# Optimization experiments

Measured on AMD Instinct MI355X. Metric: run time of the kernel, lower is better.

The kernel has to match this reference:

```python
import jax, jax.numpy as jnp
import numpy as np
from jax import lax

B, C, IC, H, W = 4, 64, 32, 64, 64


def _conv(x, w, b, stride, pad):
    y = lax.conv_general_dilated(
        x, w, (stride, stride), [(pad, pad), (pad, pad)],
        dimension_numbers=('NCHW', 'OIHW', 'NCHW'))
    return y + b[None, :, None, None]


def setup_inputs() -> dict:
    key = jax.random.key(0)
    ks = jax.random.split(key, 15)
    s = 0.05
    inp = {
        'x': jax.random.normal(ks[0], (B, C, H, W), jnp.float32),
        # GEunit convs (3x3)
        'd1_w': jax.random.normal(ks[1], (C, C, 3, 3), jnp.float32) * s,
        'd1_b': jax.random.normal(ks[2], (C,), jnp.float32) * s,
        'd2_w': jax.random.normal(ks[3], (C, C, 3, 3), jnp.float32) * s,
        'd2_b': jax.random.normal(ks[4], (C,), jnp.float32) * s,
        'd3_w': jax.random.normal(ks[5], (C, C, 3, 3), jnp.float32) * s,
        'd3_b': jax.random.normal(ks[6], (C,), jnp.float32) * s,
        # 1x1 projections
        'g_w': jax.random.normal(ks[7], (IC, C, 1, 1), jnp.float32) * s,
        'g_b': jax.random.normal(ks[8], (IC,), jnp.float32) * s,
        'th_w': jax.random.normal(ks[9], (IC, C, 1, 1), jnp.float32) * s,
        'th_b': jax.random.normal(ks[10], (IC,), jnp.float32) * s,
        'ph_w': jax.random.normal(ks[11], (IC, C, 1, 1), jnp.float32) * s,
        'ph_b': jax.random.normal(ks[12], (IC,), jnp.float32) * s,
        # output projection (zero-init in original; random here for nontrivial baseline)
        'w_w': jax.random.normal(ks[13], (C, IC, 1, 1), jnp.float32) * s,
        'w_b': jax.random.normal(ks[14], (C,), jnp.float32) * s,
    }
    return inp


def _forward(x, d1_w, d1_b, d2_w, d2_b, d3_w, d3_b,
             g_w, g_b, th_w, th_b, ph_w, ph_b, w_w, w_b):
    lrelu = lambda v: jnp.where(v >= 0, v, 0.2 * v)
    y = lrelu(_conv(x, d1_w, d1_b, 2, 1))
    y = lrelu(_conv(y, d2_w, d2_b, 2, 1))
    y = _conv(y, d3_w, d3_b, 2, 1)
    y = jax.image.resize(y, (x.shape[0], x.shape[1], x.shape[2], x.shape[3]),
                         method='bilinear')  # align_corners=False equivalent
    am = jax.nn.sigmoid(y) * x  # attention_map, [B,C,H,W]

    b, c, h, w = am.shape
    n = h * w
    g_x = _conv(am, g_w, g_b, 1, 0).reshape(b, IC, n)      # [B,IC,N]
    theta = _conv(am, th_w, th_b, 1, 0).reshape(b, IC, n)  # [B,IC,N]
    phi = _conv(am, ph_w, ph_b, 1, 0).reshape(b, IC, n)    # [B,IC,N]

    # f[b,i,j] = theta[:, i] . phi[:, j];  softmax over dim=1 (the i axis)
    f = jnp.einsum('bci,bcj->bij', theta, phi)             # [B,N,N]
    f_div_C = jax.nn.softmax(f, axis=1)
    y2 = jnp.einsum('bij,bjc->bic', f_div_C, g_x.transpose(0, 2, 1))  # [B,N,IC]
    y2 = y2.transpose(0, 2, 1).reshape(b, IC, h, w)

    W_y = _conv(y2, w_w, w_b, 1, 0)
    z = W_y + am
    return z * x


def reference(x, d1_w, d1_b, d2_w, d2_b, d3_w, d3_b,
              g_w, g_b, th_w, th_b, ph_w, ph_b, w_w, w_b):
    return _forward(x, d1_w, d1_b, d2_w, d2_b, d3_w, d3_b,
                    g_w, g_b, th_w, th_b, ph_w, ph_b, w_w, w_b)
```

## Files before the change

kernel.cpp:

```cpp
#include <hip/hip_runtime.h>

#define B_ 4
#define C_ 64
#define IC_ 32
#define N_ 4096
#define LOG2E 1.44269504088896341f

typedef __attribute__((ext_vector_type(8))) short short8;
typedef __attribute__((ext_vector_type(4))) float floatx4;
typedef unsigned short ushort_t;

__device__ __forceinline__ unsigned short f2bf(float f) {
  unsigned u = __float_as_uint(f);
  u += 0x7FFFu + ((u >> 16) & 1u);
  return (unsigned short)(u >> 16);
}
__device__ __forceinline__ float bf2f(unsigned short h) {
  return __uint_as_float(((unsigned)h) << 16);
}

__global__ void __launch_bounds__(256) pack_xw_k(
    const float* __restrict__ x, unsigned short* __restrict__ xclp,
    const float* __restrict__ d1_w, const float* __restrict__ d2_w, const float* __restrict__ d3_w,
    const float* __restrict__ th_w, const float* __restrict__ ph_w, const float* __restrict__ g_w,
    const float* __restrict__ th_b, const float* __restrict__ ph_b, const float* __restrict__ g_b,
    unsigned short* __restrict__ wpk, unsigned short* __restrict__ wproj, float* __restrict__ bproj)
{
  __shared__ float s[64][65];
  const int t = threadIdx.x;
  if (blockIdx.x < 256) {
    const int b = blockIdx.x >> 6, h = blockIdx.x & 63;
    for (int idx = t; idx < 4096; idx += 256) {
      int c = idx >> 6, w = idx & 63;
      s[c][w] = x[((size_t)(b * 64 + c)) * 4096 + h * 64 + w];
    }
    __syncthreads();
    for (int idx = t; idx < 4096; idx += 256) {
      int w = idx >> 6, c = idx & 63;
      xclp[(((size_t)b * 66 + h + 1) * 66 + (w + 1)) * 64 + c] = f2bf(s[c][w]);
    }
  } else {
    const int tid = (blockIdx.x - 256) * 256 + t;
    for (int idx = tid; idx < 3 * 36864; idx += 16 * 256) {
      int cv = idx / 36864, r = idx % 36864;
      int tap = r / 4096, r2 = r % 4096;
      int oc = r2 >> 6, ic = r2 & 63;
      const float* src = (cv == 0) ? d1_w : (cv == 1) ? d2_w : d3_w;
      wpk[(size_t)cv * 36864 + tap * 4096 + oc * 64 + ic] = f2bf(src[oc * 576 + ic * 9 + tap]);
    }
    for (int idx = tid; idx < 6144; idx += 16 * 256) {
      int m = idx >> 6, ic = idx & 63;
      float v = (m < 32) ? LOG2E * th_w[m * 64 + ic]
              : (m < 64) ? ph_w[(m - 32) * 64 + ic]
                         : g_w[(m - 64) * 64 + ic];
      wproj[m * 64 + ic] = f2bf(v);
    }
    for (int m = tid; m < 96; m += 16 * 256) {
      bproj[m] = (m < 32) ? LOG2E * th_b[m] : (m < 64) ? ph_b[m - 32] : g_b[m - 64];
    }
  }
}

template<int IN_PW, int OUT_H, bool LRELU, bool OUT_BF16>
__global__ void __launch_bounds__(64) convmf_k(
    const unsigned short* __restrict__ xin, const unsigned short* __restrict__ wp,
    const float* __restrict__ bias, unsigned short* __restrict__ obf,
    float* __restrict__ of32)
{
  constexpr int NTILES = OUT_H * OUT_H / 16;
  const int lane = threadIdx.x;
  const int n15 = lane & 15, quad = lane >> 4;
  int bx = blockIdx.x;
  const int octile = bx & 3; bx >>= 2;
  const int otile = bx % NTILES;
  const int b = bx / NTILES;
  const int o = otile * 16 + n15;
  const int oh = o / OUT_H, ow = o % OUT_H;
  const unsigned short* xb = xin + (size_t)b * IN_PW * IN_PW * 64;
  floatx4 acc = {0.f, 0.f, 0.f, 0.f};
#pragma unroll
  for (int tap = 0; tap < 9; ++tap) {
    const int kh = tap / 3, kw = tap % 3;
    const unsigned short* xpix = xb + ((size_t)(oh * 2 + kh) * IN_PW + (ow * 2 + kw)) * 64;
#pragma unroll
    for (int ks = 0; ks < 2; ++ks) {
      short8 af = *reinterpret_cast<const short8*>(
          wp + ((size_t)tap * 64 + octile * 16 + n15) * 64 + ks * 32 + quad * 8);
      short8 bf = *reinterpret_cast<const short8*>(xpix + ks * 32 + quad * 8);
      acc = __builtin_amdgcn_mfma_f32_16x16x32_bf16(af, bf, acc, 0, 0, 0);
    }
  }
  const float4 bv = *reinterpret_cast<const float4*>(bias + octile * 16 + quad * 4);
  float v[4] = {acc[0] + bv.x, acc[1] + bv.y, acc[2] + bv.z, acc[3] + bv.w};
  if (LRELU) {
#pragma unroll
    for (int r = 0; r < 4; ++r) v[r] = (v[r] >= 0.f) ? v[r] : 0.2f * v[r];
  }
  if (OUT_BF16) {
    constexpr int OPW = OUT_H + 2;
    unsigned short pk[4];
#pragma unroll
    for (int r = 0; r < 4; ++r) pk[r] = f2bf(v[r]);
    *reinterpret_cast<uint2*>(
        obf + (((size_t)b * OPW + oh + 1) * OPW + (ow + 1)) * 64 + octile * 16 + quad * 4) =
        *reinterpret_cast<uint2*>(pk);
  } else {
    *reinterpret_cast<float4*>(
        of32 + ((size_t)b * OUT_H * OUT_H + o) * 64 + octile * 16 + quad * 4) =
        *reinterpret_cast<float4*>(v);
  }
}

__global__ void __launch_bounds__(256) upsproj_k(
    const float* __restrict__ y3cl, const float* __restrict__ x,
    const unsigned short* __restrict__ wproj, const float* __restrict__ bproj,
    unsigned short* __restrict__ am_cl, unsigned short* __restrict__ thph,
    unsigned short* __restrict__ g16)
{
  const int b = blockIdx.x >> 6, oh = blockIdx.x & 63;
  const int t = threadIdx.x;
  __shared__ float s0[512], s1[512];
  __shared__ unsigned short s_am[64][72];
  float sh = (oh + 0.5f) * 0.125f - 0.5f;
  float fh = floorf(sh); float ah = sh - fh; int h0 = (int)fh;
  int h0c = min(7, max(0, h0)), h1c = min(7, max(0, h0 + 1));
  const float* yb = y3cl + (size_t)b * 4096;
  for (int i = t; i < 512; i += 256) { s0[i] = yb[h0c * 512 + i]; s1[i] = yb[h1c * 512 + i]; }
  __syncthreads();
  {
    const int ow = t >> 2, cq = t & 3;
    float sw = (ow + 0.5f) * 0.125f - 0.5f;
    float fw = floorf(sw); float aw = sw - fw; int w0 = (int)fw;
    int w0c = min(7, max(0, w0)), w1c = min(7, max(0, w0 + 1));
    const int n = oh * 64 + ow;
    const float* xb = x + (size_t)b * 64 * 4096 + n;
    unsigned short* ap = am_cl + ((size_t)b * N_ + n) * 64 + cq * 16;
#pragma unroll
    for (int u = 0; u < 4; ++u) {
      int c0 = cq * 16 + u * 4;
      float4 a00 = *reinterpret_cast<const float4*>(&s0[w0c * 64 + c0]);
      float4 a01 = *reinterpret_cast<const float4*>(&s0[w1c * 64 + c0]);
      float4 a10 = *reinterpret_cast<const float4*>(&s1[w0c * 64 + c0]);
      float4 a11 = *reinterpret_cast<const float4*>(&s1[w1c * 64 + c0]);
      float i0[4] = {a00.x * (1.f - aw) + a01.x * aw, a00.y * (1.f - aw) + a01.y * aw,
                     a00.z * (1.f - aw) + a01.z * aw, a00.w * (1.f - aw) + a01.w * aw};
      float i1[4] = {a10.x * (1.f - aw) + a11.x * aw, a10.y * (1.f - aw) + a11.y * aw,
                     a10.z * (1.f - aw) + a11.z * aw, a10.w * (1.f - aw) + a11.w * aw};
      unsigned short pk[4];
#pragma unroll
      for (int vi = 0; vi < 4; ++vi) {
        float vv = i0[vi] * (1.f - ah) + i1[vi] * ah;
        float xv = xb[(size_t)(c0 + vi) * 4096];
        float sig = 1.f / (1.f + __expf(-vv));
        pk[vi] = f2bf(sig * xv);
      }
      uint2 pkt = *reinterpret_cast<uint2*>(pk);
      *reinterpret_cast<uint2*>(ap + u * 4) = pkt;
      *reinterpret_cast<uint2*>(&s_am[ow][c0]) = pkt;
    }
  }
  __syncthreads();
  const int wave = t >> 6, lane = t & 63;
  const int n15 = lane & 15, quad = lane >> 4;
  const int n = oh * 64 + wave * 16 + n15;
  const unsigned short* srow = &s_am[wave * 16 + n15][0];
  const short8 bf0 = *reinterpret_cast<const short8*>(srow + quad * 8);
  const short8 bf1 = *reinterpret_cast<const short8*>(srow + 32 + quad * 8);
#pragma unroll
  for (int mt = 0; mt < 6; ++mt) {
    short8 a0 = *reinterpret_cast<const short8*>(wproj + ((size_t)mt * 16 + n15) * 64 + quad * 8);
    short8 a1 = *reinterpret_cast<const short8*>(wproj + ((size_t)mt * 16 + n15) * 64 + 32 + quad * 8);
    floatx4 acc = {0.f, 0.f, 0.f, 0.f};
    acc = __builtin_amdgcn_mfma_f32_16x16x32_bf16(a0, bf0, acc, 0, 0, 0);
    acc = __builtin_amdgcn_mfma_f32_16x16x32_bf16(a1, bf1, acc, 0, 0, 0);
    const float4 bv = *reinterpret_cast<const float4*>(bproj + mt * 16 + quad * 4);
    float v[4] = {acc[0] + bv.x, acc[1] + bv.y, acc[2] + bv.z, acc[3] + bv.w};
    if (mt < 4) {
      unsigned short pk[4];
#pragma unroll
      for (int r = 0; r < 4; ++r) pk[r] = f2bf(v[r]);
      *reinterpret_cast<uint2*>(thph + ((size_t)b * N_ + n) * 64 + mt * 16 + quad * 4) =
          *reinterpret_cast<uint2*>(pk);
    } else {
#pragma unroll
      for (int r = 0; r < 4; ++r)
        g16[((size_t)b * 32 + (mt - 4) * 16 + quad * 4 + r) * N_ + n] = f2bf(v[r]);
    }
  }
}

__global__ void __launch_bounds__(256) attn_stats_k(
    const unsigned short* __restrict__ thph, float* __restrict__ lpart)
{
  const int b  = blockIdx.y;
  const int iz = blockIdx.z;
  const int t = threadIdx.x, wave = t >> 6, lane = t & 63;
  const int n15 = lane & 15, quad = lane >> 4;
  const int jw = blockIdx.x * 256 + wave * 64;
  const unsigned short* base = thph + (size_t)b * N_ * 64;
  short8 bv[4];
#pragma unroll
  for (int v = 0; v < 4; ++v)
    bv[v] = *reinterpret_cast<const short8*>(base + (size_t)(jw + v * 16 + n15) * 64 + 32 + quad * 8);
  float ls[4] = {0.f, 0.f, 0.f, 0.f};
  const unsigned short* ap = base + (size_t)(iz * 256 + n15) * 64 + quad * 8;
  short8 ac = *reinterpret_cast<const short8*>(ap);
  for (int st = 0; st < 16; ++st) {
    short8 an = *reinterpret_cast<const short8*>(ap + (size_t)((st < 15) ? st + 1 : st) * 1024);
#pragma unroll
    for (int v = 0; v < 4; ++v) {
      floatx4 z = {0.f, 0.f, 0.f, 0.f};
      z = __builtin_amdgcn_mfma_f32_16x16x32_bf16(ac, bv[v], z, 0, 0, 0);
      ls[v] += (__builtin_amdgcn_exp2f(z[0]) + __builtin_amdgcn_exp2f(z[1]))
             + (__builtin_amdgcn_exp2f(z[2]) + __builtin_amdgcn_exp2f(z[3]));
    }
    ac = an;
  }
#pragma unroll
  for (int v = 0; v < 4; ++v) {
    ls[v] += __shfl_xor(ls[v], 16);
    ls[v] += __shfl_xor(ls[v], 32);
  }
  if (quad == 0) {
#pragma unroll
    for (int v = 0; v < 4; ++v)
      lpart[((size_t)iz * B_ + b) * N_ + jw + v * 16 + n15] = ls[v];
  }
}

__global__ void __launch_bounds__(256) scale_g_k(
    const float* __restrict__ lpart, unsigned short* __restrict__ g16)
{
  const int b = blockIdx.y;
  const int c0 = blockIdx.z * 8;
  const int j = blockIdx.x * 256 + threadIdx.x;
  float l = 0.f;
#pragma unroll
  for (int iz = 0; iz < 16; ++iz) l += lpart[((size_t)iz * B_ + b) * N_ + j];
  const float rl = 1.f / l;
  unsigned short* gp = g16 + ((size_t)b * 32 + c0) * N_ + j;
#pragma unroll
  for (int c = 0; c < 8; ++c) {
    gp[(size_t)c * N_] = f2bf(bf2f(gp[(size_t)c * N_]) * rl);
  }
}

#define PHI_PITCH 40
#define G_PITCH   136
__global__ void __launch_bounds__(256, 4) attn_pv_k(
    const unsigned short* __restrict__ thph, const unsigned short* __restrict__ g16,
    unsigned short* __restrict__ y2p)
{
  const int b  = blockIdx.y;
  const int jq = blockIdx.z;
  const int t = threadIdx.x, wave = t >> 6, lane = t & 63;
  const int n15 = lane & 15, quad = lane >> 4;
  const int iw = blockIdx.x * 64 + wave * 16;
  const unsigned short* base = thph + (size_t)b * N_ * 64;
  const unsigned short* gs   = g16  + (size_t)b * 32 * N_;
  __shared__ unsigned short phi_lds[2][128 * PHI_PITCH];
  __shared__ unsigned short g_lds[2][32 * G_PITCH];

  const short8 bth = *reinterpret_cast<const short8*>(base + (size_t)(iw + n15) * 64 + quad * 8);
  floatx4 Y0 = {0.f, 0.f, 0.f, 0.f}, Y1 = {0.f, 0.f, 0.f, 0.f};

  const int rphi = wave * 32 + (lane >> 2), cph = lane & 3;
  const int cg   = wave * 8  + (lane >> 4), chg = lane & 15;

  uint4 sp0, sp1, sg0, sg1;
  const int jbase = jq * 1024;
  sp0 = *reinterpret_cast<const uint4*>(base + (size_t)(jbase + rphi) * 64 + 32 + cph * 8);
  sp1 = *reinterpret_cast<const uint4*>(base + (size_t)(jbase + rphi + 16) * 64 + 32 + cph * 8);
  sg0 = *reinterpret_cast<const uint4*>(gs + (size_t)cg * N_ + jbase + chg * 8);
  sg1 = *reinterpret_cast<const uint4*>(gs + (size_t)(cg + 4) * N_ + jbase + chg * 8);
  *reinterpret_cast<uint4*>(&phi_lds[0][rphi * PHI_PITCH + cph * 8]) = sp0;
  *reinterpret_cast<uint4*>(&phi_lds[0][(rphi + 16) * PHI_PITCH + cph * 8]) = sp1;
  *reinterpret_cast<uint4*>(&g_lds[0][cg * G_PITCH + chg * 8]) = sg0;
  *reinterpret_cast<uint4*>(&g_lds[0][(cg + 4) * G_PITCH + chg * 8]) = sg1;
  __syncthreads();

  int j0 = jbase;
  for (int ch = 0; ch < 8; ++ch, j0 += 128) {
    const int cur = ch & 1;
    if (ch < 7) {
      const int jn = j0 + 128;
      sp0 = *reinterpret_cast<const uint4*>(base + (size_t)(jn + rphi) * 64 + 32 + cph * 8);
      sp1 = *reinterpret_cast<const uint4*>(base + (size_t)(jn + rphi + 16) * 64 + 32 + cph * 8);
      sg0 = *reinterpret_cast<const uint4*>(gs + (size_t)cg * N_ + jn + chg * 8);
      sg1 = *reinterpret_cast<const uint4*>(gs + (size_t)(cg + 4) * N_ + jn + chg * 8);
    }
    const unsigned short* phb = &phi_lds[cur][0];
    const unsigned short* glb = &g_lds[cur][0];
    unsigned pk[8][2];
#pragma unroll
    for (int jt = 0; jt < 8; ++jt) {
      short8 aph = *reinterpret_cast<const short8*>(phb + (jt * 16 + n15) * PHI_PITCH + quad * 8);
      floatx4 z = {0.f, 0.f, 0.f, 0.f};
      z = __builtin_amdgcn_mfma_f32_16x16x32_bf16(aph, bth, z, 0, 0, 0);
      float e0 = __builtin_amdgcn_exp2f(z[0]), e1 = __builtin_amdgcn_exp2f(z[1]);
      float e2 = __builtin_amdgcn_exp2f(z[2]), e3 = __builtin_amdgcn_exp2f(z[3]);
      pk[jt][0] = __builtin_amdgcn_perm(__float_as_uint(e1), __float_as_uint(e0), 0x07060302);
      pk[jt][1] = __builtin_amdgcn_perm(__float_as_uint(e3), __float_as_uint(e2), 0x07060302);
    }
#pragma unroll
    for (int sg = 0; sg < 4; ++sg) {
      union { unsigned u[4]; short8 v; } pa, gb0, gb1;
      pa.u[0] = pk[2 * sg][0];     pa.u[1] = pk[2 * sg][1];
      pa.u[2] = pk[2 * sg + 1][0]; pa.u[3] = pk[2 * sg + 1][1];
      const unsigned short* gr0 = glb + n15 * G_PITCH + sg * 32 + quad * 4;
      const unsigned short* gr1 = glb + (16 + n15) * G_PITCH + sg * 32 + quad * 4;
      uint2 lo0 = *reinterpret_cast<const uint2*>(gr0);
      uint2 hi0 = *reinterpret_cast<const uint2*>(gr0 + 16);
      uint2 lo1 = *reinterpret_cast<const uint2*>(gr1);
      uint2 hi1 = *reinterpret_cast<const uint2*>(gr1 + 16);
      gb0.u[0] = lo0.x; gb0.u[1] = lo0.y; gb0.u[2] = hi0.x; gb0.u[3] = hi0.y;
      gb1.u[0] = lo1.x; gb1.u[1] = lo1.y; gb1.u[2] = hi1.x; gb1.u[3] = hi1.y;
      Y0 = __builtin_amdgcn_mfma_f32_16x16x32_bf16(pa.v, gb0.v, Y0, 0, 0, 0);
      Y1 = __builtin_amdgcn_mfma_f32_16x16x32_bf16(pa.v, gb1.v, Y1, 0, 0, 0);
    }
    if (ch < 7) {
      const int nb = cur ^ 1;
      *reinterpret_cast<uint4*>(&phi_lds[nb][rphi * PHI_PITCH + cph * 8]) = sp0;
      *reinterpret_cast<uint4*>(&phi_lds[nb][(rphi + 16) * PHI_PITCH + cph * 8]) = sp1;
      *reinterpret_cast<uint4*>(&g_lds[nb][cg * G_PITCH + chg * 8]) = sg0;
      *reinterpret_cast<uint4*>(&g_lds[nb][(cg + 4) * G_PITCH + chg * 8]) = sg1;
    }
    __syncthreads();
  }
  unsigned w0[2], w1[2];
  w0[0] = ((unsigned)f2bf(Y0[1]) << 16) | f2bf(Y0[0]);
  w0[1] = ((unsigned)f2bf(Y0[3]) << 16) | f2bf(Y0[2]);
  w1[0] = ((unsigned)f2bf(Y1[1]) << 16) | f2bf(Y1[0]);
  w1[1] = ((unsigned)f2bf(Y1[3]) << 16) | f2bf(Y1[2]);
  *reinterpret_cast<uint2*>(
      y2p + (((size_t)jq * B_ + b) * 32 + n15) * N_ + iw + quad * 4) =
      *reinterpret_cast<uint2*>(w0);
  *reinterpret_cast<uint2*>(
      y2p + (((size_t)jq * B_ + b) * 32 + 16 + n15) * N_ + iw + quad * 4) =
      *reinterpret_cast<uint2*>(w1);
}

__global__ void __launch_bounds__(256) final_k(
    const unsigned short* __restrict__ y2p, const float* __restrict__ w_w,
    const float* __restrict__ w_b, const unsigned short* __restrict__ am_cl,
    const float* __restrict__ x, float* __restrict__ out)
{
  const int n0 = (blockIdx.x * 256 + threadIdx.x) * 2;
  const int o0 = blockIdx.y * 8;
  const int b  = blockIdx.z;
  float a0[8], a1[8];
#pragma unroll
  for (int u = 0; u < 8; ++u) { a0[u] = w_b[o0 + u]; a1[u] = a0[u]; }
  for (int c = 0; c < 32; ++c) {
    float s0 = 0.f, s1 = 0.f;
#pragma unroll
    for (int ph = 0; ph < 4; ++ph) {
      unsigned v = *reinterpret_cast<const unsigned*>(
          y2p + (((size_t)ph * B_ + b) * 32 + c) * N_ + n0);
      s0 += bf2f((unsigned short)(v & 0xffffu));
      s1 += bf2f((unsigned short)(v >> 16));
    }
#pragma unroll
    for (int u = 0; u < 8; ++u) {
      float wv = w_w[(o0 + u) * 32 + c];
      a0[u] += wv * s0; a1[u] += wv * s1;
    }
  }
  const short8 am0 = *reinterpret_cast<const short8*>(am_cl + ((size_t)b * N_ + n0) * 64 + o0);
  const short8 am1 = *reinterpret_cast<const short8*>(am_cl + ((size_t)b * N_ + n0 + 1) * 64 + o0);
#pragma unroll
  for (int u = 0; u < 8; ++u) {
    size_t off = ((size_t)b * 64 + o0 + u) * N_ + n0;
    float2 xv = *reinterpret_cast<const float2*>(x + off);
    float2 ov;
    ov.x = (a0[u] + bf2f((unsigned short)am0[u])) * xv.x;
    ov.y = (a1[u] + bf2f((unsigned short)am1[u])) * xv.y;
    *reinterpret_cast<float2*>(out + off) = ov;
  }
}

extern "C" void kernel_launch(void* const* d_in, const int* in_sizes, int n_in,
                              void* d_out, int out_size, void* d_ws, size_t ws_size,
                              hipStream_t stream) {
  const float* x    = (const float*)d_in[0];
  const float* d1_w = (const float*)d_in[1];
  const float* d1_b = (const float*)d_in[2];
  const float* d2_w = (const float*)d_in[3];
  const float* d2_b = (const float*)d_in[4];
  const float* d3_w = (const float*)d_in[5];
  const float* d3_b = (const float*)d_in[6];
  const float* g_w  = (const float*)d_in[7];
  const float* g_b  = (const float*)d_in[8];
  const float* th_w = (const float*)d_in[9];
  const float* th_b = (const float*)d_in[10];
  const float* ph_w = (const float*)d_in[11];
  const float* ph_b = (const float*)d_in[12];
  const float* w_w  = (const float*)d_in[13];
  const float* w_b  = (const float*)d_in[14];
  float* out = (float*)d_out;

  char* p = (char*)d_ws;
  unsigned short* am_cl = (unsigned short*)p;  p += (size_t)B_ * N_ * 64 * 2;
  unsigned short* thph  = (unsigned short*)p;  p += (size_t)B_ * N_ * 64 * 2;
  unsigned short* g16   = (unsigned short*)p;  p += (size_t)B_ * 32 * N_ * 2;
  float* lpart          = (float*)p;           p += (size_t)16 * B_ * N_ * 4;
  unsigned short* y2p   = (unsigned short*)p;  p += (size_t)4 * B_ * 32 * N_ * 2;
  float* y3cl           = (float*)p;           p += (size_t)B_ * 64 * 64 * 4;
  unsigned short* wpk   = (unsigned short*)p;  p += (size_t)3 * 36864 * 2;
  unsigned short* wproj = (unsigned short*)p;  p += (size_t)96 * 64 * 2;
  float* bproj          = (float*)p;           p += (size_t)96 * 4;
  char* zbase = p;
  unsigned short* xclp  = (unsigned short*)p;  p += (size_t)B_ * 66 * 66 * 64 * 2;
  unsigned short* y1clp = (unsigned short*)p;  p += (size_t)B_ * 34 * 34 * 64 * 2;
  unsigned short* y2clp = (unsigned short*)p;  p += (size_t)B_ * 18 * 18 * 64 * 2;
  const size_t zbytes = (size_t)(p - zbase);

  hipMemsetAsync(zbase, 0, zbytes, stream);
  pack_xw_k<<<272, 256, 0, stream>>>(x, xclp, d1_w, d2_w, d3_w, th_w, ph_w, g_w,
                                     th_b, ph_b, g_b, wpk, wproj, bproj);
  convmf_k<66, 32, true,  true ><<<1024, 64, 0, stream>>>(xclp,  wpk,             d1_b, y1clp, nullptr);
  convmf_k<34, 16, true,  true ><<<256,  64, 0, stream>>>(y1clp, wpk + 36864,     d2_b, y2clp, nullptr);
  convmf_k<18,  8, false, false><<<64,   64, 0, stream>>>(y2clp, wpk + 2 * 36864, d3_b, nullptr, y3cl);
  upsproj_k<<<256, 256, 0, stream>>>(y3cl, x, wproj, bproj, am_cl, thph, g16);
  attn_stats_k<<<dim3(16, 4, 16), 256, 0, stream>>>(thph, lpart);
  scale_g_k<<<dim3(16, 4, 4), 256, 0, stream>>>(lpart, g16);
  attn_pv_k<<<dim3(64, 4, 4), 256, 0, stream>>>(thph, g16, y2p);
  final_k<<<dim3(8, 8, 4), 256, 0, stream>>>(y2p, w_w, w_b, am_cl, x, out);
}
```

Before: 153.8 us.

## Split conv K across waves with LDS reduction; stage theta tile in LDS

```diff
diff --git a/kernel.cpp b/kernel.cpp
--- a/kernel.cpp
+++ b/kernel.cpp
@@ -8,7 +8,6 @@
 
 typedef __attribute__((ext_vector_type(8))) short short8;
 typedef __attribute__((ext_vector_type(4))) float floatx4;
-typedef unsigned short ushort_t;
 
 __device__ __forceinline__ unsigned short f2bf(float f) {
   unsigned u = __float_as_uint(f);
@@ -62,18 +61,17 @@
 }
 
 template<int IN_PW, int OUT_H, bool LRELU, bool OUT_BF16>
-__global__ void __launch_bounds__(64) convmf_k(
+__global__ void __launch_bounds__(512) convmf_k(
     const unsigned short* __restrict__ xin, const unsigned short* __restrict__ wp,
     const float* __restrict__ bias, unsigned short* __restrict__ obf,
     float* __restrict__ of32)
 {
   constexpr int NTILES = OUT_H * OUT_H / 16;
-  const int lane = threadIdx.x;
+  const int t = threadIdx.x, lane = t & 63, wave = t >> 6;
+  const int octile = wave & 3, ks = wave >> 2;
   const int n15 = lane & 15, quad = lane >> 4;
-  int bx = blockIdx.x;
-  const int octile = bx & 3; bx >>= 2;
-  const int otile = bx % NTILES;
-  const int b = bx / NTILES;
+  const int otile = blockIdx.x % NTILES;
+  const int b = blockIdx.x / NTILES;
   const int o = otile * 16 + n15;
   const int oh = o / OUT_H, ow = o % OUT_H;
   const unsigned short* xb = xin + (size_t)b * IN_PW * IN_PW * 64;
@@ -82,32 +80,38 @@
   for (int tap = 0; tap < 9; ++tap) {
     const int kh = tap / 3, kw = tap % 3;
     const unsigned short* xpix = xb + ((size_t)(oh * 2 + kh) * IN_PW + (ow * 2 + kw)) * 64;
-#pragma unroll
-    for (int ks = 0; ks < 2; ++ks) {
-      short8 af = *reinterpret_cast<const short8*>(
-          wp + ((size_t)tap * 64 + octile * 16 + n15) * 64 + ks * 32 + quad * 8);
-      short8 bf = *reinterpret_cast<const short8*>(xpix + ks * 32 + quad * 8);
-      acc = __builtin_amdgcn_mfma_f32_16x16x32_bf16(af, bf, acc, 0, 0, 0);
-    }
-  }
-  const float4 bv = *reinterpret_cast<const float4*>(bias + octile * 16 + quad * 4);
-  float v[4] = {acc[0] + bv.x, acc[1] + bv.y, acc[2] + bv.z, acc[3] + bv.w};
-  if (LRELU) {
-#pragma unroll
-    for (int r = 0; r < 4; ++r) v[r] = (v[r] >= 0.f) ? v[r] : 0.2f * v[r];
-  }
-  if (OUT_BF16) {
-    constexpr int OPW = OUT_H + 2;
-    unsigned short pk[4];
-#pragma unroll
-    for (int r = 0; r < 4; ++r) pk[r] = f2bf(v[r]);
-    *reinterpret_cast<uint2*>(
-        obf + (((size_t)b * OPW + oh + 1) * OPW + (ow + 1)) * 64 + octile * 16 + quad * 4) =
-        *reinterpret_cast<uint2*>(pk);
-  } else {
-    *reinterpret_cast<float4*>(
-        of32 + ((size_t)b * OUT_H * OUT_H + o) * 64 + octile * 16 + quad * 4) =
-        *reinterpret_cast<float4*>(v);
+    short8 af = *reinterpret_cast<const short8*>(
+        wp + ((size_t)tap * 64 + octile * 16 + n15) * 64 + ks * 32 + quad * 8);
+    short8 bf = *reinterpret_cast<const short8*>(xpix + ks * 32 + quad * 8);
+    acc = __builtin_amdgcn_mfma_f32_16x16x32_bf16(af, bf, acc, 0, 0, 0);
+  }
+  __shared__ float red[4][64][4];
+  if (ks == 1) {
+#pragma unroll
+    for (int r = 0; r < 4; ++r) red[octile][lane][r] = acc[r];
+  }
+  __syncthreads();
+  if (ks == 0) {
+    const float4 bv = *reinterpret_cast<const float4*>(bias + octile * 16 + quad * 4);
+    float v[4];
+#pragma unroll
+    for (int r = 0; r < 4; ++r) {
+      v[r] = acc[r] + red[octile][lane][r] + ((const float*)&bv)[r];
+      if (LRELU) v[r] = (v[r] >= 0.f) ? v[r] : 0.2f * v[r];
+    }
+    if (OUT_BF16) {
+      constexpr int OPW = OUT_H + 2;
+      unsigned short pk[4];
+#pragma unroll
+      for (int r = 0; r < 4; ++r) pk[r] = f2bf(v[r]);
+      *reinterpret_cast<uint2*>(
+          obf + (((size_t)b * OPW + oh + 1) * OPW + (ow + 1)) * 64 + octile * 16 + quad * 4) =
+          *reinterpret_cast<uint2*>(pk);
+    } else {
+      *reinterpret_cast<float4*>(
+          of32 + ((size_t)b * OUT_H * OUT_H + o) * 64 + octile * 16 + quad * 4) =
+          *reinterpret_cast<float4*>(v);
+    }
   }
 }
 
@@ -189,6 +193,7 @@
   }
 }
 
+#define TH_PITCH 40
 __global__ void __launch_bounds__(256) attn_stats_k(
     const unsigned short* __restrict__ thph, float* __restrict__ lpart)
 {
@@ -198,15 +203,24 @@
   const int n15 = lane & 15, quad = lane >> 4;
   const int jw = blockIdx.x * 256 + wave * 64;
   const unsigned short* base = thph + (size_t)b * N_ * 64;
+  __shared__ unsigned short th[256 * TH_PITCH];
+#pragma unroll
+  for (int it = 0; it < 4; ++it) {
+    int idx = it * 256 + t;
+    int row = idx >> 2, ck = idx & 3;
+    *reinterpret_cast<uint4*>(&th[row * TH_PITCH + ck * 8]) =
+        *reinterpret_cast<const uint4*>(base + (size_t)(iz * 256 + row) * 64 + ck * 8);
+  }
   short8 bv[4];
 #pragma unroll
   for (int v = 0; v < 4; ++v)
     bv[v] = *reinterpret_cast<const short8*>(base + (size_t)(jw + v * 16 + n15) * 64 + 32 + quad * 8);
+  __syncthreads();
   float ls[4] = {0.f, 0.f, 0.f, 0.f};
-  const unsigned short* ap = base + (size_t)(iz * 256 + n15) * 64 + quad * 8;
-  short8 ac = *reinterpret_cast<const short8*>(ap);
+  short8 ac = *reinterpret_cast<const short8*>(&th[n15 * TH_PITCH + quad * 8]);
   for (int st = 0; st < 16; ++st) {
-    short8 an = *reinterpret_cast<const short8*>(ap + (size_t)((st < 15) ? st + 1 : st) * 1024);
+    const int rn = ((st < 15) ? st + 1 : st) * 16 + n15;
+    short8 an = *reinterpret_cast<const short8*>(&th[rn * TH_PITCH + quad * 8]);
 #pragma unroll
     for (int v = 0; v < 4; ++v) {
       floatx4 z = {0.f, 0.f, 0.f, 0.f};
@@ -418,9 +432,9 @@
   hipMemsetAsync(zbase, 0, zbytes, stream);
   pack_xw_k<<<272, 256, 0, stream>>>(x, xclp, d1_w, d2_w, d3_w, th_w, ph_w, g_w,
                                      th_b, ph_b, g_b, wpk, wproj, bproj);
-  convmf_k<66, 32, true,  true ><<<1024, 64, 0, stream>>>(xclp,  wpk,             d1_b, y1clp, nullptr);
-  convmf_k<34, 16, true,  true ><<<256,  64, 0, stream>>>(y1clp, wpk + 36864,     d2_b, y2clp, nullptr);
-  convmf_k<18,  8, false, false><<<64,   64, 0, stream>>>(y2clp, wpk + 2 * 36864, d3_b, nullptr, y3cl);
+  convmf_k<66, 32, true,  true ><<<256, 512, 0, stream>>>(xclp,  wpk,             d1_b, y1clp, nullptr);
+  convmf_k<34, 16, true,  true ><<<64,  512, 0, stream>>>(y1clp, wpk + 36864,     d2_b, y2clp, nullptr);
+  convmf_k<18,  8, false, false><<<16,  512, 0, stream>>>(y2clp, wpk + 2 * 36864, d3_b, nullptr, y3cl);
   upsproj_k<<<256, 256, 0, stream>>>(y3cl, x, wproj, bproj, am_cl, thph, g16);
   attn_stats_k<<<dim3(16, 4, 16), 256, 0, stream>>>(thph, lpart);
   scale_g_k<<<dim3(16, 4, 4), 256, 0, stream>>>(lpart, g16);
```

New measurement: 160.3 us. +4.2%, slower.

## Fuse attention stats, g scaling and PV into one persistent kernel with grid barriers

Applied to the files above, without the earlier changes.

```diff
diff --git a/kernel.cpp b/kernel.cpp
--- a/kernel.cpp
+++ b/kernel.cpp
@@ -5,10 +5,10 @@
 #define IC_ 32
 #define N_ 4096
 #define LOG2E 1.44269504088896341f
+#define AGENT_SCOPE __HIP_MEMORY_SCOPE_AGENT
 
 typedef __attribute__((ext_vector_type(8))) short short8;
 typedef __attribute__((ext_vector_type(4))) float floatx4;
-typedef unsigned short ushort_t;
 
 __device__ __forceinline__ unsigned short f2bf(float f) {
   unsigned u = __float_as_uint(f);
@@ -19,12 +19,24 @@
   return __uint_as_float(((unsigned)h) << 16);
 }
 
+__device__ __forceinline__ void grid_barrier(unsigned* cnt, unsigned target) {
+  __syncthreads();
+  if (threadIdx.x == 0) {
+    __hip_atomic_fetch_add(cnt, 1u, __ATOMIC_ACQ_REL, AGENT_SCOPE);
+    while (__hip_atomic_load(cnt, __ATOMIC_ACQUIRE, AGENT_SCOPE) < target)
+      __builtin_amdgcn_s_sleep(2);
+  }
+  __syncthreads();
+}
+
 __global__ void __launch_bounds__(256) pack_xw_k(
     const float* __restrict__ x, unsigned short* __restrict__ xclp,
+    unsigned short* __restrict__ y1clp, unsigned short* __restrict__ y2clp,
     const float* __restrict__ d1_w, const float* __restrict__ d2_w, const float* __restrict__ d3_w,
     const float* __restrict__ th_w, const float* __restrict__ ph_w, const float* __restrict__ g_w,
     const float* __restrict__ th_b, const float* __restrict__ ph_b, const float* __restrict__ g_b,
-    unsigned short* __restrict__ wpk, unsigned short* __restrict__ wproj, float* __restrict__ bproj)
+    unsigned short* __restrict__ wpk, unsigned short* __restrict__ wproj, float* __restrict__ bproj,
+    unsigned* __restrict__ bar)
 {
   __shared__ float s[64][65];
   const int t = threadIdx.x;
@@ -41,6 +53,7 @@
     }
   } else {
     const int tid = (blockIdx.x - 256) * 256 + t;
+    if (tid < 2) bar[tid] = 0;
     for (int idx = tid; idx < 3 * 36864; idx += 16 * 256) {
       int cv = idx / 36864, r = idx % 36864;
       int tap = r / 4096, r2 = r % 4096;
@@ -57,6 +70,22 @@
     }
     for (int m = tid; m < 96; m += 16 * 256) {
       bproj[m] = (m < 32) ? LOG2E * th_b[m] : (m < 64) ? ph_b[m - 32] : g_b[m - 64];
+    }
+#pragma unroll
+    for (int img = 0; img < 3; ++img) {
+      const int P = (img == 0) ? 66 : (img == 1) ? 34 : 18;
+      unsigned short* dst = (img == 0) ? xclp : (img == 1) ? y1clp : y2clp;
+      const int ring = 2 * P + 2 * (P - 2);
+      const int tot = B_ * ring * 64;
+      for (int idx = tid; idx < tot; idx += 16 * 256) {
+        int c = idx & 63, r = idx >> 6;
+        int k = r % ring, b = r / ring;
+        int h, w;
+        if (k < P)          { h = 0;     w = k; }
+        else if (k < 2 * P) { h = P - 1; w = k - P; }
+        else { int q = k - 2 * P; h = 1 + (q >> 1); w = (q & 1) ? (P - 1) : 0; }
+        dst[(((size_t)b * P + h) * P + w) * 64 + c] = 0;
+      }
     }
   }
 }
@@ -189,155 +218,157 @@
   }
 }
 
-__global__ void __launch_bounds__(256) attn_stats_k(
-    const unsigned short* __restrict__ thph, float* __restrict__ lpart)
+#define TH_PITCH 40
+#define PHI_PITCH 40
+#define G_PITCH   136
+union MegaLds {
+  unsigned short th[256 * TH_PITCH];
+  struct {
+    unsigned short phi[2][128 * PHI_PITCH];
+    unsigned short g[2][32 * G_PITCH];
+  } c;
+};
+
+__global__ void __launch_bounds__(1024) attn_mega_k(
+    const unsigned short* __restrict__ thph, unsigned short* g16,
+    float* lpart, unsigned short* __restrict__ y2p, unsigned* bar)
 {
-  const int b  = blockIdx.y;
-  const int iz = blockIdx.z;
+  __shared__ MegaLds L;
+  const int bid = blockIdx.x;
   const int t = threadIdx.x, wave = t >> 6, lane = t & 63;
   const int n15 = lane & 15, quad = lane >> 4;
-  const int jw = blockIdx.x * 256 + wave * 64;
-  const unsigned short* base = thph + (size_t)b * N_ * 64;
-  short8 bv[4];
-#pragma unroll
-  for (int v = 0; v < 4; ++v)
-    bv[v] = *reinterpret_cast<const short8*>(base + (size_t)(jw + v * 16 + n15) * 64 + 32 + quad * 8);
-  float ls[4] = {0.f, 0.f, 0.f, 0.f};
-  const unsigned short* ap = base + (size_t)(iz * 256 + n15) * 64 + quad * 8;
-  short8 ac = *reinterpret_cast<const short8*>(ap);
-  for (int st = 0; st < 16; ++st) {
-    short8 an = *reinterpret_cast<const short8*>(ap + (size_t)((st < 15) ? st + 1 : st) * 1024);
+
+  {
+    const int b = bid & 3, iz = (bid >> 2) & 15, jq = bid >> 6;
+    const unsigned short* base = thph + (size_t)b * N_ * 64;
+    {
+      const int row = t >> 2, ck = t & 3;
+      *reinterpret_cast<uint4*>(&L.th[row * TH_PITCH + ck * 8]) =
+          *reinterpret_cast<const uint4*>(base + (size_t)(iz * 256 + row) * 64 + ck * 8);
+    }
+    const int jw = jq * 1024 + wave * 64;
+    short8 bv[4];
+#pragma unroll
+    for (int v = 0; v < 4; ++v)
+      bv[v] = *reinterpret_cast<const short8*>(base + (size_t)(jw + v * 16 + n15) * 64 + 32 + quad * 8);
+    __syncthreads();
+    float ls[4] = {0.f, 0.f, 0.f, 0.f};
+    short8 ac = *reinterpret_cast<const short8*>(&L.th[n15 * TH_PITCH + quad * 8]);
+    for (int st = 0; st < 16; ++st) {
+      const int rn = ((st < 15) ? st + 1 : st) * 16 + n15;
+      short8 an = *reinterpret_cast<const short8*>(&L.th[rn * TH_PITCH + quad * 8]);
+#pragma unroll
+      for (int v = 0; v < 4; ++v) {
+        floatx4 z = {0.f, 0.f, 0.f, 0.f};
+        z = __builtin_amdgcn_mfma_f32_16x16x32_bf16(ac, bv[v], z, 0, 0, 0);
+        ls[v] += (__builtin_amdgcn_exp2f(z[0]) + __builtin_amdgcn_exp2f(z[1]))
+               + (__builtin_amdgcn_exp2f(z[2]) + __builtin_amdgcn_exp2f(z[3]));
+      }
+      ac = an;
+    }
 #pragma unroll
     for (int v = 0; v < 4; ++v) {
-      floatx4 z = {0.f, 0.f, 0.f, 0.f};
-      z = __builtin_amdgcn_mfma_f32_16x16x32_bf16(ac, bv[v], z, 0, 0, 0);
-      ls[v] += (__builtin_amdgcn_exp2f(z[0]) + __builtin_amdgcn_exp2f(z[1]))
-             + (__builtin_amdgcn_exp2f(z[2]) + __builtin_amdgcn_exp2f(z[3]));
-    }
-    ac = an;
-  }
-#pragma unroll
-  for (int v = 0; v < 4; ++v) {
-    ls[v] += __shfl_xor(ls[v], 16);
-    ls[v] += __shfl_xor(ls[v], 32);
-  }
-  if (quad == 0) {
-#pragma unroll
-    for (int v = 0; v < 4; ++v)
-      lpart[((size_t)iz * B_ + b) * N_ + jw + v * 16 + n15] = ls[v];
-  }
-}
-
-__global__ void __launch_bounds__(256) scale_g_k(
-    const float* __restrict__ lpart, unsigned short* __restrict__ g16)
-{
-  const int b = blockIdx.y;
-  const int c0 = blockIdx.z * 8;
-  const int j = blockIdx.x * 256 + threadIdx.x;
-  float l = 0.f;
-#pragma unroll
-  for (int iz = 0; iz < 16; ++iz) l += lpart[((size_t)iz * B_ + b) * N_ + j];
-  const float rl = 1.f / l;
-  unsigned short* gp = g16 + ((size_t)b * 32 + c0) * N_ + j;
-#pragma unroll
-  for (int c = 0; c < 8; ++c) {
-    gp[(size_t)c * N_] = f2bf(bf2f(gp[(size_t)c * N_]) * rl);
-  }
-}
-
-#define PHI_PITCH 40
-#define G_PITCH   136
-__global__ void __launch_bounds__(256, 4) attn_pv_k(
-    const unsigned short* __restrict__ thph, const unsigned short* __restrict__ g16,
-    unsigned short* __restrict__ y2p)
-{
-  const int b  = blockIdx.y;
-  const int jq = blockIdx.z;
-  const int t = threadIdx.x, wave = t >> 6, lane = t & 63;
-  const int n15 = lane & 15, quad = lane >> 4;
-  const int iw = blockIdx.x * 64 + wave * 16;
-  const unsigned short* base = thph + (size_t)b * N_ * 64;
-  const unsigned short* gs   = g16  + (size_t)b * 32 * N_;
-  __shared__ unsigned short phi_lds[2][128 * PHI_PITCH];
-  __shared__ unsigned short g_lds[2][32 * G_PITCH];
-
-  const short8 bth = *reinterpret_cast<const short8*>(base + (size_t)(iw + n15) * 64 + quad * 8);
-  floatx4 Y0 = {0.f, 0.f, 0.f, 0.f}, Y1 = {0.f, 0.f, 0.f, 0.f};
-
-  const int rphi = wave * 32 + (lane >> 2), cph = lane & 3;
-  const int cg   = wave * 8  + (lane >> 4), chg = lane & 15;
-
-  uint4 sp0, sp1, sg0, sg1;
-  const int jbase = jq * 1024;
-  sp0 = *reinterpret_cast<const uint4*>(base + (size_t)(jbase + rphi) * 64 + 32 + cph * 8);
-  sp1 = *reinterpret_cast<const uint4*>(base + (size_t)(jbase + rphi + 16) * 64 + 32 + cph * 8);
-  sg0 = *reinterpret_cast<const uint4*>(gs + (size_t)cg * N_ + jbase + chg * 8);
-  sg1 = *reinterpret_cast<const uint4*>(gs + (size_t)(cg + 4) * N_ + jbase + chg * 8);
-  *reinterpret_cast<uint4*>(&phi_lds[0][rphi * PHI_PITCH + cph * 8]) = sp0;
-  *reinterpret_cast<uint4*>(&phi_lds[0][(rphi + 16) * PHI_PITCH + cph * 8]) = sp1;
-  *reinterpret_cast<uint4*>(&g_lds[0][cg * G_PITCH + chg * 8]) = sg0;
-  *reinterpret_cast<uint4*>(&g_lds[0][(cg + 4) * G_PITCH + chg * 8]) = sg1;
-  __syncthreads();
-
-  int j0 = jbase;
-  for (int ch = 0; ch < 8; ++ch, j0 += 128) {
-    const int cur = ch & 1;
-    if (ch < 7) {
-      const int jn = j0 + 128;
-      sp0 = *reinterpret_cast<const uint4*>(base + (size_t)(jn + rphi) * 64 + 32 + cph * 8);
-      sp1 = *reinterpret_cast<const uint4*>(base + (size_t)(jn + rphi + 16) * 64 + 32 + cph * 8);
-      sg0 = *reinterpret_cast<const uint4*>(gs + (size_t)cg * N_ + jn + chg * 8);
-      sg1 = *reinterpret_cast<const uint4*>(gs + (size_t)(cg + 4) * N_ + jn + chg * 8);
-    }
-    const unsigned short* phb = &phi_lds[cur][0];
-    const unsigned short* glb = &g_lds[cur][0];
-    unsigned pk[8][2];
-#pragma unroll
-    for (int jt = 0; jt < 8; ++jt) {
-      short8 aph = *reinterpret_cast<const short8*>(phb + (jt * 16 + n15) * PHI_PITCH + quad * 8);
-      floatx4 z = {0.f, 0.f, 0.f, 0.f};
-      z = __builtin_amdgcn_mfma_f32_16x16x32_bf16(aph, bth, z, 0, 0, 0);
-      float e0 = __builtin_amdgcn_exp2f(z[0]), e1 = __builtin_amdgcn_exp2f(z[1]);
-      float e2 = __builtin_amdgcn_exp2f(z[2]), e3 = __builtin_amdgcn_exp2f(z[3]);
-      pk[jt][0] = __builtin_amdgcn_perm(__float_as_uint(e1), __float_as_uint(e0), 0x07060302);
-      pk[jt][1] = __builtin_amdgcn_perm(__float_as_uint(e3), __float_as_uint(e2), 0x07060302);
-    }
-#pragma unroll
-    for (int sg = 0; sg < 4; ++sg) {
-      union { unsigned u[4]; short8 v; } pa, gb0, gb1;
-      pa.u[0] = pk[2 * sg][0];     pa.u[1] = pk[2 * sg][1];
-      pa.u[2] = pk[2 * sg + 1][0]; pa.u[3] = pk[2 * sg + 1][1];
-      const unsigned short* gr0 = glb + n15 * G_PITCH + sg * 32 + quad * 4;
-      const unsigned short* gr1 = glb + (16 + n15) * G_PITCH + sg * 32 + quad * 4;
-      uint2 lo0 = *reinterpret_cast<const uint2*>(gr0);
-      uint2 hi0 = *reinterpret_cast<const uint2*>(gr0 + 16);
-      uint2 lo1 = *reinterpret_cast<const uint2*>(gr1);
-      uint2 hi1 = *reinterpret_cast<const uint2*>(gr1 + 16);
-      gb0.u[0] = lo0.x; gb0.u[1] = lo0.y; gb0.u[2] = hi0.x; gb0.u[3] = hi0.y;
-      gb1.u[0] = lo1.x; gb1.u[1] = lo1.y; gb1.u[2] = hi1.x; gb1.u[3] = hi1.y;
-      Y0 = __builtin_amdgcn_mfma_f32_16x16x32_bf16(pa.v, gb0.v, Y0, 0, 0, 0);
-      Y1 = __builtin_amdgcn_mfma_f32_16x16x32_bf16(pa.v, gb1.v, Y1, 0, 0, 0);
-    }
-    if (ch < 7) {
-      const int nb = cur ^ 1;
-      *reinterpret_cast<uint4*>(&phi_lds[nb][rphi * PHI_PITCH + cph * 8]) = sp0;
-      *reinterpret_cast<uint4*>(&phi_lds[nb][(rphi + 16) * PHI_PITCH + cph * 8]) = sp1;
-      *reinterpret_cast<uint4*>(&g_lds[nb][cg * G_PITCH + chg * 8]) = sg0;
-      *reinterpret_cast<uint4*>(&g_lds[nb][(cg + 4) * G_PITCH + chg * 8]) = sg1;
-    }
+      ls[v] += __shfl_xor(ls[v], 16);
+      ls[v] += __shfl_xor(ls[v], 32);
+    }
+    if (quad == 0) {
+#pragma unroll
+      for (int v = 0; v < 4; ++v)
+        lpart[((size_t)iz * B_ + b) * N_ + jw + v * 16 + n15] = ls[v];
+    }
+  }
+  grid_barrier(&bar[0], 256);
+
+  {
+    const int b = bid & 3;
+    const int j = (bid >> 2) * 64 + (t & 63);
+    const int cg = t >> 6;
+    float l = 0.f;
+#pragma unroll
+    for (int iz = 0; iz < 16; ++iz) l += lpart[((size_t)iz * B_ + b) * N_ + j];
+    const float rl = 1.f / l;
+    unsigned short* gp = g16 + ((size_t)b * 32 + cg * 2) * N_ + j;
+    gp[0]  = f2bf(bf2f(gp[0]) * rl);
+    gp[N_] = f2bf(bf2f(gp[N_]) * rl);
+  }
+  grid_barrier(&bar[1], 256);
+
+  {
+    const int b = bid & 3, jq = (bid >> 2) & 3, ig = bid >> 4;
+    const unsigned short* base = thph + (size_t)b * N_ * 64;
+    const unsigned short* gs   = g16  + (size_t)b * 32 * N_;
+    const int iw = ig * 256 + wave * 16;
+    const short8 bth = *reinterpret_cast<const short8*>(base + (size_t)(iw + n15) * 64 + quad * 8);
+    floatx4 Y0 = {0.f, 0.f, 0.f, 0.f}, Y1 = {0.f, 0.f, 0.f, 0.f};
+
+    const bool isphi = t < 512;
+    const int pr = (t & 511) >> 2, pseg = t & 3;
+    const int gc = (t & 511) >> 4, gseg = t & 15;
+    const int jbase = jq * 1024;
+
+    uint4 s;
+    if (isphi) s = *reinterpret_cast<const uint4*>(base + (size_t)(jbase + pr) * 64 + 32 + pseg * 8);
+    else       s = *reinterpret_cast<const uint4*>(gs + (size_t)gc * N_ + jbase + gseg * 8);
+    if (isphi) *reinterpret_cast<uint4*>(&L.c.phi[0][pr * PHI_PITCH + pseg * 8]) = s;
+    else       *reinterpret_cast<uint4*>(&L.c.g[0][gc * G_PITCH + gseg * 8]) = s;
     __syncthreads();
-  }
-  unsigned w0[2], w1[2];
-  w0[0] = ((unsigned)f2bf(Y0[1]) << 16) | f2bf(Y0[0]);
-  w0[1] = ((unsigned)f2bf(Y0[3]) << 16) | f2bf(Y0[2]);
-  w1[0] = ((unsigned)f2bf(Y1[1]) << 16) | f2bf(Y1[0]);
-  w1[1] = ((unsigned)f2bf(Y1[3]) << 16) | f2bf(Y1[2]);
-  *reinterpret_cast<uint2*>(
-      y2p + (((size_t)jq * B_ + b) * 32 + n15) * N_ + iw + quad * 4) =
-      *reinterpret_cast<uint2*>(w0);
-  *reinterpret_cast<uint2*>(
-      y2p + (((size_t)jq * B_ + b) * 32 + 16 + n15) * N_ + iw + quad * 4) =
-      *reinterpret_cast<uint2*>(w1);
+
+    int j0 = jbase;
+    for (int ch = 0; ch < 8; ++ch, j0 += 128) {
+      const int cur = ch & 1;
+      if (ch < 7) {
+        const int jn = j0 + 128;
+        if (isphi) s = *reinterpret_cast<const uint4*>(base + (size_t)(jn + pr) * 64 + 32 + pseg * 8);
+        else       s = *reinterpret_cast<const uint4*>(gs + (size_t)gc * N_ + jn + gseg * 8);
+      }
+      const unsigned short* phb = &L.c.phi[cur][0];
+      const unsigned short* glb = &L.c.g[cur][0];
+      unsigned pk[8][2];
+#pragma unroll
+      for (int jt = 0; jt < 8; ++jt) {
+        short8 aph = *reinterpret_cast<const short8*>(phb + (jt * 16 + n15) * PHI_PITCH + quad * 8);
+        floatx4 z = {0.f, 0.f, 0.f, 0.f};
+        z = __builtin_amdgcn_mfma_f32_16x16x32_bf16(aph, bth, z, 0, 0, 0);
+        float e0 = __builtin_amdgcn_exp2f(z[0]), e1 = __builtin_amdgcn_exp2f(z[1]);
+        float e2 = __builtin_amdgcn_exp2f(z[2]), e3 = __builtin_amdgcn_exp2f(z[3]);
+        pk[jt][0] = __builtin_amdgcn_perm(__float_as_uint(e1), __float_as_uint(e0), 0x07060302);
+        pk[jt][1] = __builtin_amdgcn_perm(__float_as_uint(e3), __float_as_uint(e2), 0x07060302);
+      }
+#pragma unroll
+      for (int sg = 0; sg < 4; ++sg) {
+        union { unsigned u[4]; short8 v; } pa, gb0, gb1;
+        pa.u[0] = pk[2 * sg][0];     pa.u[1] = pk[2 * sg][1];
+        pa.u[2] = pk[2 * sg + 1][0]; pa.u[3] = pk[2 * sg + 1][1];
+        const unsigned short* gr0 = glb + n15 * G_PITCH + sg * 32 + quad * 4;
+        const unsigned short* gr1 = glb + (16 + n15) * G_PITCH + sg * 32 + quad * 4;
+        uint2 lo0 = *reinterpret_cast<const uint2*>(gr0);
+        uint2 hi0 = *reinterpret_cast<const uint2*>(gr0 + 16);
+        uint2 lo1 = *reinterpret_cast<const uint2*>(gr1);
+        uint2 hi1 = *reinterpret_cast<const uint2*>(gr1 + 16);
+        gb0.u[0] = lo0.x; gb0.u[1] = lo0.y; gb0.u[2] = hi0.x; gb0.u[3] = hi0.y;
+        gb1.u[0] = lo1.x; gb1.u[1] = lo1.y; gb1.u[2] = hi1.x; gb1.u[3] = hi1.y;
+        Y0 = __builtin_amdgcn_mfma_f32_16x16x32_bf16(pa.v, gb0.v, Y0, 0, 0, 0);
+        Y1 = __builtin_amdgcn_mfma_f32_16x16x32_bf16(pa.v, gb1.v, Y1, 0, 0, 0);
+      }
+      if (ch < 7) {
+        const int nb = cur ^ 1;
+        if (isphi) *reinterpret_cast<uint4*>(&L.c.phi[nb][pr * PHI_PITCH + pseg * 8]) = s;
+        else       *reinterpret_cast<uint4*>(&L.c.g[nb][gc * G_PITCH + gseg * 8]) = s;
+      }
+      __syncthreads();
+    }
+    unsigned w0[2], w1[2];
+    w0[0] = ((unsigned)f2bf(Y0[1]) << 16) | f2bf(Y0[0]);
+    w0[1] = ((unsigned)f2bf(Y0[3]) << 16) | f2bf(Y0[2]);
+    w1[0] = ((unsigned)f2bf(Y1[1]) << 16) | f2bf(Y1[0]);
+    w1[1] = ((unsigned)f2bf(Y1[3]) << 16) | f2bf(Y1[2]);
+    *reinterpret_cast<uint2*>(
+        y2p + (((size_t)jq * B_ + b) * 32 + n15) * N_ + iw + quad * 4) =
+        *reinterpret_cast<uint2*>(w0);
+    *reinterpret_cast<uint2*>(
+        y2p + (((size_t)jq * B_ + b) * 32 + 16 + n15) * N_ + iw + quad * 4) =
+        *reinterpret_cast<uint2*>(w1);
+  }
 }
 
 __global__ void __launch_bounds__(256) final_k(
@@ -409,21 +440,18 @@
   unsigned short* wpk   = (unsigned short*)p;  p += (size_t)3 * 36864 * 2;
   unsigned short* wproj = (unsigned short*)p;  p += (size_t)96 * 64 * 2;
   float* bproj          = (float*)p;           p += (size_t)96 * 4;
-  char* zbase = p;
+  unsigned* bar         = (unsigned*)p;        p += 256;
   unsigned short* xclp  = (unsigned short*)p;  p += (size_t)B_ * 66 * 66 * 64 * 2;
   unsigned short* y1clp = (unsigned short*)p;  p += (size_t)B_ * 34 * 34 * 64 * 2;
   unsigned short* y2clp = (unsigned short*)p;  p += (size_t)B_ * 18 * 18 * 64 * 2;
-  const size_t zbytes = (size_t)(p - zbase);
-
-  hipMemsetAsync(zbase, 0, zbytes, stream);
-  pack_xw_k<<<272, 256, 0, stream>>>(x, xclp, d1_w, d2_w, d3_w, th_w, ph_w, g_w,
-                                     th_b, ph_b, g_b, wpk, wproj, bproj);
+
+  pack_xw_k<<<272, 256, 0, stream>>>(x, xclp, y1clp, y2clp,
+                                     d1_w, d2_w, d3_w, th_w, ph_w, g_w,
+                                     th_b, ph_b, g_b, wpk, wproj, bproj, bar);
   convmf_k<66, 32, true,  true ><<<1024, 64, 0, stream>>>(xclp,  wpk,             d1_b, y1clp, nullptr);
   convmf_k<34, 16, true,  true ><<<256,  64, 0, stream>>>(y1clp, wpk + 36864,     d2_b, y2clp, nullptr);
   convmf_k<18,  8, false, false><<<64,   64, 0, stream>>>(y2clp, wpk + 2 * 36864, d3_b, nullptr, y3cl);
   upsproj_k<<<256, 256, 0, stream>>>(y3cl, x, wproj, bproj, am_cl, thph, g16);
-  attn_stats_k<<<dim3(16, 4, 16), 256, 0, stream>>>(thph, lpart);
-  scale_g_k<<<dim3(16, 4, 4), 256, 0, stream>>>(lpart, g16);
-  attn_pv_k<<<dim3(64, 4, 4), 256, 0, stream>>>(thph, g16, y2p);
+  attn_mega_k<<<256, 1024, 0, stream>>>(thph, g16, lpart, y2p, bar);
   final_k<<<dim3(8, 8, 4), 256, 0, stream>>>(y2p, w_w, w_b, am_cl, x, out);
 }
```

Measured after the change: 178.8 us. 16.2% more time.

## Fold softmax normalization into PV kernel, drop memset and scale_g launch

Applied to the files above, without the earlier changes.

```diff
diff --git a/kernel.cpp b/kernel.cpp
--- a/kernel.cpp
+++ b/kernel.cpp
@@ -8,7 +8,6 @@
 
 typedef __attribute__((ext_vector_type(8))) short short8;
 typedef __attribute__((ext_vector_type(4))) float floatx4;
-typedef unsigned short ushort_t;
 
 __device__ __forceinline__ unsigned short f2bf(float f) {
   unsigned u = __float_as_uint(f);
@@ -21,6 +20,7 @@
 
 __global__ void __launch_bounds__(256) pack_xw_k(
     const float* __restrict__ x, unsigned short* __restrict__ xclp,
+    unsigned short* __restrict__ y1clp, unsigned short* __restrict__ y2clp,
     const float* __restrict__ d1_w, const float* __restrict__ d2_w, const float* __restrict__ d3_w,
     const float* __restrict__ th_w, const float* __restrict__ ph_w, const float* __restrict__ g_w,
     const float* __restrict__ th_b, const float* __restrict__ ph_b, const float* __restrict__ g_b,
@@ -57,6 +57,22 @@
     }
     for (int m = tid; m < 96; m += 16 * 256) {
       bproj[m] = (m < 32) ? LOG2E * th_b[m] : (m < 64) ? ph_b[m - 32] : g_b[m - 64];
+    }
+#pragma unroll
+    for (int img = 0; img < 3; ++img) {
+      const int P = (img == 0) ? 66 : (img == 1) ? 34 : 18;
+      unsigned short* dst = (img == 0) ? xclp : (img == 1) ? y1clp : y2clp;
+      const int ring = 2 * P + 2 * (P - 2);
+      const int tot = B_ * ring * 64;
+      for (int idx = tid; idx < tot; idx += 16 * 256) {
+        int c = idx & 63, r = idx >> 6;
+        int k = r % ring, b = r / ring;
+        int h, w;
+        if (k < P)          { h = 0;     w = k; }
+        else if (k < 2 * P) { h = P - 1; w = k - P; }
+        else { int q = k - 2 * P; h = 1 + (q >> 1); w = (q & 1) ? (P - 1) : 0; }
+        dst[(((size_t)b * P + h) * P + w) * 64 + c] = 0;
+      }
     }
   }
 }
@@ -192,11 +208,13 @@
 __global__ void __launch_bounds__(256) attn_stats_k(
     const unsigned short* __restrict__ thph, float* __restrict__ lpart)
 {
-  const int b  = blockIdx.y;
-  const int iz = blockIdx.z;
+  const int bid = blockIdx.x;
+  const int b  = bid & 3;
+  const int iz = (bid >> 2) & 15;
+  const int jgrp = bid >> 6;
   const int t = threadIdx.x, wave = t >> 6, lane = t & 63;
   const int n15 = lane & 15, quad = lane >> 4;
-  const int jw = blockIdx.x * 256 + wave * 64;
+  const int jw = jgrp * 256 + wave * 64;
   const unsigned short* base = thph + (size_t)b * N_ * 64;
   short8 bv[4];
 #pragma unroll
@@ -228,38 +246,24 @@
   }
 }
 
-__global__ void __launch_bounds__(256) scale_g_k(
-    const float* __restrict__ lpart, unsigned short* __restrict__ g16)
-{
-  const int b = blockIdx.y;
-  const int c0 = blockIdx.z * 8;
-  const int j = blockIdx.x * 256 + threadIdx.x;
-  float l = 0.f;
-#pragma unroll
-  for (int iz = 0; iz < 16; ++iz) l += lpart[((size_t)iz * B_ + b) * N_ + j];
-  const float rl = 1.f / l;
-  unsigned short* gp = g16 + ((size_t)b * 32 + c0) * N_ + j;
-#pragma unroll
-  for (int c = 0; c < 8; ++c) {
-    gp[(size_t)c * N_] = f2bf(bf2f(gp[(size_t)c * N_]) * rl);
-  }
-}
-
 #define PHI_PITCH 40
 #define G_PITCH   136
 __global__ void __launch_bounds__(256, 4) attn_pv_k(
     const unsigned short* __restrict__ thph, const unsigned short* __restrict__ g16,
-    unsigned short* __restrict__ y2p)
-{
-  const int b  = blockIdx.y;
-  const int jq = blockIdx.z;
+    const float* __restrict__ lpart, unsigned short* __restrict__ y2p)
+{
+  const int bid = blockIdx.x;
+  const int b  = bid & 3;
+  const int jq = (bid >> 2) & 3;
+  const int itile = bid >> 4;
   const int t = threadIdx.x, wave = t >> 6, lane = t & 63;
   const int n15 = lane & 15, quad = lane >> 4;
-  const int iw = blockIdx.x * 64 + wave * 16;
+  const int iw = itile * 64 + wave * 16;
   const unsigned short* base = thph + (size_t)b * N_ * 64;
   const unsigned short* gs   = g16  + (size_t)b * 32 * N_;
   __shared__ unsigned short phi_lds[2][128 * PHI_PITCH];
   __shared__ unsigned short g_lds[2][32 * G_PITCH];
+  __shared__ unsigned short s_linv[1024];
 
   const short8 bth = *reinterpret_cast<const short8*>(base + (size_t)(iw + n15) * 64 + quad * 8);
   floatx4 Y0 = {0.f, 0.f, 0.f, 0.f}, Y1 = {0.f, 0.f, 0.f, 0.f};
@@ -273,6 +277,19 @@
   sp1 = *reinterpret_cast<const uint4*>(base + (size_t)(jbase + rphi + 16) * 64 + 32 + cph * 8);
   sg0 = *reinterpret_cast<const uint4*>(gs + (size_t)cg * N_ + jbase + chg * 8);
   sg1 = *reinterpret_cast<const uint4*>(gs + (size_t)(cg + 4) * N_ + jbase + chg * 8);
+  {
+    float4 acc = {0.f, 0.f, 0.f, 0.f};
+#pragma unroll
+    for (int iz = 0; iz < 16; ++iz) {
+      float4 lp = *reinterpret_cast<const float4*>(
+          lpart + ((size_t)iz * B_ + b) * N_ + jbase + t * 4);
+      acc.x += lp.x; acc.y += lp.y; acc.z += lp.z; acc.w += lp.w;
+    }
+    unsigned short pk[4];
+    pk[0] = f2bf(1.f / acc.x); pk[1] = f2bf(1.f / acc.y);
+    pk[2] = f2bf(1.f / acc.z); pk[3] = f2bf(1.f / acc.w);
+    *reinterpret_cast<uint2*>(&s_linv[t * 4]) = *reinterpret_cast<uint2*>(pk);
+  }
   *reinterpret_cast<uint4*>(&phi_lds[0][rphi * PHI_PITCH + cph * 8]) = sp0;
   *reinterpret_cast<uint4*>(&phi_lds[0][(rphi + 16) * PHI_PITCH + cph * 8]) = sp1;
   *reinterpret_cast<uint4*>(&g_lds[0][cg * G_PITCH + chg * 8]) = sg0;
@@ -297,8 +314,11 @@
       short8 aph = *reinterpret_cast<const short8*>(phb + (jt * 16 + n15) * PHI_PITCH + quad * 8);
       floatx4 z = {0.f, 0.f, 0.f, 0.f};
       z = __builtin_amdgcn_mfma_f32_16x16x32_bf16(aph, bth, z, 0, 0, 0);
-      float e0 = __builtin_amdgcn_exp2f(z[0]), e1 = __builtin_amdgcn_exp2f(z[1]);
-      float e2 = __builtin_amdgcn_exp2f(z[2]), e3 = __builtin_amdgcn_exp2f(z[3]);
+      uint2 lv = *reinterpret_cast<const uint2*>(&s_linv[ch * 128 + jt * 16 + quad * 4]);
+      float l0 = bf2f((unsigned short)(lv.x & 0xffffu)), l1 = bf2f((unsigned short)(lv.x >> 16));
+      float l2 = bf2f((unsigned short)(lv.y & 0xffffu)), l3 = bf2f((unsigned short)(lv.y >> 16));
+      float e0 = __builtin_amdgcn_exp2f(z[0]) * l0, e1 = __builtin_amdgcn_exp2f(z[1]) * l1;
+      float e2 = __builtin_amdgcn_exp2f(z[2]) * l2, e3 = __builtin_amdgcn_exp2f(z[3]) * l3;
       pk[jt][0] = __builtin_amdgcn_perm(__float_as_uint(e1), __float_as_uint(e0), 0x07060302);
       pk[jt][1] = __builtin_amdgcn_perm(__float_as_uint(e3), __float_as_uint(e2), 0x07060302);
     }
@@ -409,21 +429,18 @@
   unsigned short* wpk   = (unsigned short*)p;  p += (size_t)3 * 36864 * 2;
   unsigned short* wproj = (unsigned short*)p;  p += (size_t)96 * 64 * 2;
   float* bproj          = (float*)p;           p += (size_t)96 * 4;
-  char* zbase = p;
   unsigned short* xclp  = (unsigned short*)p;  p += (size_t)B_ * 66 * 66 * 64 * 2;
   unsigned short* y1clp = (unsigned short*)p;  p += (size_t)B_ * 34 * 34 * 64 * 2;
   unsigned short* y2clp = (unsigned short*)p;  p += (size_t)B_ * 18 * 18 * 64 * 2;
-  const size_t zbytes = (size_t)(p - zbase);
-
-  hipMemsetAsync(zbase, 0, zbytes, stream);
-  pack_xw_k<<<272, 256, 0, stream>>>(x, xclp, d1_w, d2_w, d3_w, th_w, ph_w, g_w,
+
+  pack_xw_k<<<272, 256, 0, stream>>>(x, xclp, y1clp, y2clp,
+                                     d1_w, d2_w, d3_w, th_w, ph_w, g_w,
                                      th_b, ph_b, g_b, wpk, wproj, bproj);
   convmf_k<66, 32, true,  true ><<<1024, 64, 0, stream>>>(xclp,  wpk,             d1_b, y1clp, nullptr);
   convmf_k<34, 16, true,  true ><<<256,  64, 0, stream>>>(y1clp, wpk + 36864,     d2_b, y2clp, nullptr);
   convmf_k<18,  8, false, false><<<64,   64, 0, stream>>>(y2clp, wpk + 2 * 36864, d3_b, nullptr, y3cl);
   upsproj_k<<<256, 256, 0, stream>>>(y3cl, x, wproj, bproj, am_cl, thph, g16);
-  attn_stats_k<<<dim3(16, 4, 16), 256, 0, stream>>>(thph, lpart);
-  scale_g_k<<<dim3(16, 4, 4), 256, 0, stream>>>(lpart, g16);
-  attn_pv_k<<<dim3(64, 4, 4), 256, 0, stream>>>(thph, g16, y2p);
+  attn_stats_k<<<1024, 256, 0, stream>>>(thph, lpart);
+  attn_pv_k<<<1024, 256, 0, stream>>>(thph, g16, lpart, y2p);
   final_k<<<dim3(8, 8, 4), 256, 0, stream>>>(y2p, w_w, w_b, am_cl, x, out);
 }
```

Result: slower. 160.1 us (+4.1%).
